# Kernel optimization log

Measured on AMD Instinct MI355X. Metric: run time of the kernel, lower is better.

Reference implementation:

```python
import jax, jax.numpy as jnp
import numpy as np

N, K, C0, H = 256, 16, 16, 32  # vertices, regular degree, input feats, hidden


def setup_inputs() -> dict:
    key = jax.random.key(0)
    ks = jax.random.split(key, 4)
    # k-regular circulant graph: neighbors of i are i+/-1..i+/-K//2 (mod N), sorted by vertex id
    offs = np.concatenate([np.arange(1, K // 2 + 1), -np.arange(1, K // 2 + 1)])
    nbrs = np.sort((np.arange(N)[:, None] + offs[None, :]) % N, axis=1).astype(np.int32)
    X = jax.random.normal(ks[0], (N, C0), jnp.float32)
    W1 = jax.random.normal(ks[1], (18 * C0, H), jnp.float32) / np.sqrt(18 * C0)
    b1 = jnp.zeros((H,), jnp.float32)
    W2 = jax.random.normal(ks[2], (18 * H, H), jnp.float32) / np.sqrt(18 * H)
    b2 = jnp.zeros((H,), jnp.float32)
    fc_w = jax.random.normal(ks[3], (H, 1), jnp.float32) / np.sqrt(H)
    fc_b = jnp.zeros((1,), jnp.float32)
    return {"X": X, "nbrs": jnp.asarray(nbrs), "W1": W1, "b1": b1,
            "W2": W2, "b2": b2, "fc_w": fc_w, "fc_b": fc_b}


def contract18(T, A):
    """All 18 contractions of F6[t,a,b,e,f,c] = T[t,a,b,c] * A[e,f],
    exactly matching _collapse6to3 (_c6to2_111 + _c6to2_12 + _c6to2_3),
    without materializing the 6-d tensor.
    T: (n, k, k, k, c) with axes (vertex, t, a, b, channel); A: (k, k).
    Returns (n, k, k, 18*c)."""
    S = A.sum()            # total sum of A
    r = A.sum(1)           # row sums
    tr = jnp.trace(A)
    sum_b = T.sum(3)              # (n,t,a,c)
    sum_t = T.sum(1)              # (n,a,b,c)
    sum_ab = T.sum((2, 3))        # (n,t,c)
    sum_tb = T.sum((1, 3))        # (n,a,c)
    sum_all = T.sum((1, 2, 3))    # (n,c)
    # _c6to2_111 (5 permutations)
    c1 = sum_b * S
    c2 = sum_ab[:, :, None, :] * r[None, None, :, None]
    c3 = sum_t * S
    c4 = sum_tb[:, :, None, :] * r[None, None, :, None]
    c5 = sum_all[:, None, None, :] * A[None, :, :, None]
    # _c6to2_12 (1 nontrivial permutation + 9 identical identity permutations)
    c6 = jnp.einsum('ntabc,b->ntac', T, r)
    c7 = sum_b * tr  # repeated 9 times, as in the source
    # _c6to2_3 (3 planar-diagonal contractions)
    d_ab = jnp.diagonal(T, axis1=2, axis2=3).transpose(0, 1, 3, 2)   # (n,t,a,c): T[t,a,a,c]
    c16 = jnp.einsum('ntac,ea->ntec', d_ab, A)
    d_tb = jnp.diagonal(T, axis1=1, axis2=3)                          # (n,a,c,t): T[t,a,t,c]
    c17 = jnp.einsum('nact,et->naec', d_tb, A)
    d_ttt = jnp.einsum('ntttc->ntc', T).sum(1)                        # (n,c)
    c18 = d_ttt[:, None, None, :] * A[None, :, :, None]
    return jnp.concatenate([c1, c2, c3, c4, c5, c6] + [c7] * 9 + [c16, c17, c18], axis=-1)


def _forward(X, nbrs, W1, b1, W2, b2, fc_w, fc_b):
    n, k = nbrs.shape
    # chi_{i,t}[a,p] = 1 iff a-th neighbor of i == p-th neighbor of j, j = nbrs[i,t]
    NN = nbrs[nbrs]                                                    # (n,k,k)
    CH = (nbrs[:, None, :, None] == NN[:, :, None, :]).astype(X.dtype)  # (n,t,a,p)
    A = jnp.eye(k, dtype=X.dtype)  # chi_{i,i} is the k x k identity for every i

    # get_F0: broadcast vertex features to (n, k, k, c0)
    F = jnp.broadcast_to(X[:, None, None, :], (n, k, k, X.shape[1]))

    def layer(F, W, b):
        Fg = F[nbrs]                                             # (n,t,p,q,c) gather neighbor features
        tmp = jnp.einsum('ntap,ntpqc->ntaqc', CH, Fg)            # chi @ F
        T = jnp.einsum('ntaqc,ntbq->ntabc', tmp, CH)             # (chi @ F) @ chi^T
        col = contract18(T, A)                                   # (n,k,k,18c)
        return jax.nn.relu(col @ W + b)

    F1 = layer(F, W1, b1)
    F2 = layer(F1, W2, b2)
    # get_Troot then full sum: chi_root scatters F2 entries injectively into [n,n,c],
    # so sum over Troot == sum over all entries of F2.
    g = F2.sum((0, 1, 2))                                        # (H,)
    return g @ fc_w + fc_b                                       # (1,)


def reference(X, nbrs, W1, b1, W2, b2, fc_w, fc_b):
    return _forward(X, nbrs, W1, b1, W2, b2, fc_w, fc_b)
```

## Files before the change

### kernel.cpp

```cpp
#include <hip/hip_runtime.h>


constexpr int KN = 16, HH = 32, NV = 256, C2 = 32;

typedef float f32x2 __attribute__((ext_vector_type(2)));
typedef float f32x4 __attribute__((ext_vector_type(4)));

__device__ __forceinline__ f32x2 pkfma(f32x2 a, f32x2 b, f32x2 c) {
    f32x2 d;
    asm("v_pk_fma_f32 %0, %1, %2, %3" : "=v"(d) : "v"(a), "v"(b), "v"(c));
    return d;
}
__device__ __forceinline__ f32x2 pkadd(f32x2 a, f32x2 b) {
    f32x2 d;
    asm("v_pk_add_f32 %0, %1, %2" : "=v"(d) : "v"(a), "v"(b));
    return d;
}
__device__ __forceinline__ f32x2 pkmul(f32x2 a, f32x2 b) {
    f32x2 d;
    asm("v_pk_mul_f32 %0, %1, %2" : "=v"(d) : "v"(a), "v"(b));
    return d;
}
__device__ __forceinline__ f32x2 vlo(f32x4 v) { return __builtin_shufflevector(v, v, 0, 1); }
__device__ __forceinline__ f32x2 vhi(f32x4 v) { return __builtin_shufflevector(v, v, 2, 3); }

#define MM_DS(WLDS, NC, COEF_EXPR, ACC2) do {                                  \
    const f32x4* W4_ = (const f32x4*)(WLDS);                                   \
    _Pragma("unroll")                                                          \
    for (int ci = 0; ci < (NC); ++ci) {                                        \
        const float cfs_ = (COEF_EXPR);                                        \
        const f32x2 cf2_ = {cfs_, cfs_};                                       \
        _Pragma("unroll")                                                      \
        for (int h4 = 0; h4 < 8; ++h4) {                                       \
            const f32x4 w_ = W4_[ci * 8 + h4];                                 \
            (ACC2)[2*h4+0] = pkfma(cf2_, vlo(w_), (ACC2)[2*h4+0]);             \
            (ACC2)[2*h4+1] = pkfma(cf2_, vhi(w_), (ACC2)[2*h4+1]);             \
        }                                                                      \
    }                                                                          \
} while (0)

__global__ __launch_bounds__(512)
void ccn_l1(const float* __restrict__ X, const int* __restrict__ nbrs,
            const float* __restrict__ W1, const float* __restrict__ bias,
            float* __restrict__ F1c, float* __restrict__ outz,
            const float* __restrict__ W2f, float* __restrict__ Wsb2)
{
    __shared__ float sE1[6 * 512];
    __shared__ float sPP2[8 * 256 * 4];
    __shared__ float sX[16][20];
    __shared__ float sV[16][164];
    __shared__ int   s_nbi[16];
    __shared__ int   s_nbj[16][17];
    __shared__ int   s_P[16][16];
    __shared__ int   s_vm[16];
    __shared__ float s_m[16];

    const int tid  = threadIdx.x;
    const int i    = ((blockIdx.x & 7) << 5) | (blockIdx.x >> 3);

    if (blockIdx.x == 0 && tid == 0) outz[0] = 0.f;

    if (blockIdx.x < 2) {
        const int u = (blockIdx.x << 9) | tid;
        float acc = 0.f;
        #pragma unroll
        for (int g = 6; g < 15; ++g) acc += W2f[g * 1024 + u];
        Wsb2[u] = 16.f * W2f[u] + W2f[5 * 1024 + u] + 16.f * acc;
    }

    if (tid < 16) s_nbi[tid] = nbrs[i * 16 + tid];
    __syncthreads();

    if (tid < 256) {
        const int t = tid >> 4, y = tid & 15;
        const int j = s_nbi[t];
        s_nbj[t][y] = nbrs[j * 16 + y];
        sX[t][y]    = X[j * 16 + y];
    } else {
        const int u = tid - 256;
        float acc = 0.f;
        #pragma unroll
        for (int g = 6; g < 15; ++g) acc += W1[g * 512 + u];
        sE1[u]        = 16.f * W1[u] + W1[5 * 512 + u] + 16.f * acc;
        sE1[512 + u]  = W1[512 + u];
        sE1[1024 + u] = W1[15 * 512 + u];
        sE1[1536 + u] = W1[2 * 512 + u];
        sE1[2048 + u] = W1[3 * 512 + u];
        sE1[2560 + u] = W1[4 * 512 + u];
    }
    __syncthreads();

    if (tid < 256) {
        const int t = tid >> 4, y = tid & 15;
        const int tgt = s_nbi[y];
        int p = -1;
        #pragma unroll
        for (int q = 0; q < 16; ++q) if (s_nbj[t][q] == tgt) p = q;
        s_P[t][y] = p;
        unsigned long long bal = __ballot(p >= 0);
        if (y == 0) {
            int vm = (int)((bal >> ((t & 3) * 16)) & 0xFFFFull);
            s_vm[t] = vm;
            s_m[t]  = (float)__popc(vm);
        }
    } else {
        const int u = tid;
        float acc = 0.f;
        #pragma unroll
        for (int g = 6; g < 15; ++g) acc += W1[g * 512 + u];
        sE1[u]        = 16.f * W1[u] + W1[5 * 512 + u] + 16.f * acc;
        sE1[512 + u]  = W1[512 + u];
        sE1[1024 + u] = W1[15 * 512 + u];
        sE1[1536 + u] = W1[2 * 512 + u];
        sE1[2048 + u] = W1[3 * 512 + u];
        sE1[2560 + u] = W1[4 * 512 + u];
    }
    __syncthreads();

    if (tid < 256) {
        const int t = tid >> 4, y = tid & 15, x = t;
        float Y0[16];
        #pragma unroll
        for (int c4 = 0; c4 < 4; ++c4) {
            float4 v = *(const float4*)&sX[t][4 * c4];
            Y0[4*c4+0] = v.x; Y0[4*c4+1] = v.y; Y0[4*c4+2] = v.z; Y0[4*c4+3] = v.w;
        }
        f32x2 Z42[8], Z52[8];
        #pragma unroll
        for (int c = 0; c < 8; ++c) { Z42[c] = (f32x2){0.f,0.f}; Z52[c] = (f32x2){0.f,0.f}; }
        #pragma unroll
        for (int tp = 0; tp < 16; ++tp) {
            const int vm = s_vm[tp];
            const float mt = s_m[tp];
            const float fb = ((vm >> x) & 1) ? mt : 0.f;
            const float f5 = mt * mt;
            const f32x2 fb2 = {fb, fb};
            const f32x2 f52 = {f5, f5};
            #pragma unroll
            for (int c4 = 0; c4 < 4; ++c4) {
                const f32x4 v = *(const f32x4*)&sX[tp][4 * c4];
                Z42[2*c4+0] = pkfma(fb2, vlo(v), Z42[2*c4+0]);
                Z42[2*c4+1] = pkfma(fb2, vhi(v), Z42[2*c4+1]);
                Z52[2*c4+0] = pkfma(f52, vlo(v), Z52[2*c4+0]);
                Z52[2*c4+1] = pkfma(f52, vhi(v), Z52[2*c4+1]);
            }
        }
        const float m = s_m[t];
        float v0a=0.f,v0b=0.f,v1a=0.f,v1b=0.f,v2a=0.f,v2b=0.f;
        float v3a=0.f,v3b=0.f,v4a=0.f,v4b=0.f;
        const float2* Wsb = (const float2*)(sE1 + 0 * 512);
        const float2* Wab = (const float2*)(sE1 + 1 * 512);
        const float2* W16 = (const float2*)(sE1 + 2 * 512);
        const float2* Wtb = (const float2*)(sE1 + 4 * 512);
        const float2* Wal = (const float2*)(sE1 + 5 * 512);
        #pragma unroll
        for (int c = 0; c < 16; ++c) {
            const float cf0 = m * Y0[c];
            const float cf1 = m * cf0;
            const float cf2 = Y0[c];
            const float cf3 = Z42[c >> 1][c & 1];
            const float cf4 = Z52[c >> 1][c & 1];
            const int idx = c * 16 + y;
            float2 w0 = Wsb[idx]; v0a = fmaf(cf0, w0.x, v0a); v0b = fmaf(cf0, w0.y, v0b);
            float2 w1 = Wab[idx]; v1a = fmaf(cf1, w1.x, v1a); v1b = fmaf(cf1, w1.y, v1b);
            float2 w2 = W16[idx]; v2a = fmaf(cf2, w2.x, v2a); v2b = fmaf(cf2, w2.y, v2b);
            float2 w3 = Wtb[idx]; v3a = fmaf(cf3, w3.x, v3a); v3b = fmaf(cf3, w3.y, v3b);
            float2 w4 = Wal[idx]; v4a = fmaf(cf4, w4.x, v4a); v4b = fmaf(cf4, w4.y, v4b);
        }
        *(float2*)&sV[t][0 * 32 + 2 * y] = make_float2(v0a, v0b);
        *(float2*)&sV[t][1 * 32 + 2 * y] = make_float2(v1a, v1b);
        *(float2*)&sV[t][2 * 32 + 2 * y] = make_float2(v2a, v2b);
        *(float2*)&sV[t][3 * 32 + 2 * y] = make_float2(v3a, v3b);
        *(float2*)&sV[t][4 * 32 + 2 * y] = make_float2(v4a, v4b);
    } else {
        const int w = tid - 256;
        const int t = w >> 4, y = w & 15, x = t;
        f32x2 Z22[8];
        #pragma unroll
        for (int c = 0; c < 8; ++c) Z22[c] = (f32x2){0.f,0.f};
        #pragma unroll
        for (int tp = 0; tp < 16; ++tp) {
            const int vm = s_vm[tp];
            const float f2 = (float)((vm >> x) & (vm >> y) & 1);
            const f32x2 f22 = {f2, f2};
            #pragma unroll
            for (int c4 = 0; c4 < 4; ++c4) {
                const f32x4 v = *(const f32x4*)&sX[tp][4 * c4];
                Z22[2*c4+0] = pkfma(f22, vlo(v), Z22[2*c4+0]);
                Z22[2*c4+1] = pkfma(f22, vhi(v), Z22[2*c4+1]);
            }
        }
        f32x2 pp2[16];
        #pragma unroll
        for (int h = 0; h < 16; ++h) pp2[h] = (f32x2){0.f,0.f};
        MM_DS(sE1 + 3 * 512, 16, 16.f * Z22[ci >> 1][ci & 1], pp2);
        const int cell = y * 16 + t;
        #pragma unroll
        for (int h4 = 0; h4 < 8; ++h4) {
            const int base = (h4 * 256 + cell) * 4;
            *(f32x2*)&sPP2[base]     = pp2[2*h4+0];
            *(f32x2*)&sPP2[base + 2] = pp2[2*h4+1];
        }
    }
    __syncthreads();

    if (tid < 256) {
        const int q = tid >> 4, p = tid & 15;
        const float vy  = (s_P[p][q] >= 0) ? 1.f : 0.f;
        const float dxy = (p == q) ? 1.f : 0.f;
        const f32x2 vy2 = {vy, vy}, dxy2 = {dxy, dxy};
        float4* F4 = (float4*)F1c;
        const size_t basec = ((size_t)i * 16 + q) * 128 + p;
        #pragma unroll
        for (int h4 = 0; h4 < 8; ++h4) {
            const f32x4 V0 = *(const f32x4*)&sV[p][0 * 32 + 4 * h4];
            const f32x4 V1 = *(const f32x4*)&sV[p][1 * 32 + 4 * h4];
            const f32x4 V2 = *(const f32x4*)&sV[p][2 * 32 + 4 * h4];
            const f32x4 V3 = *(const f32x4*)&sV[p][3 * 32 + 4 * h4];
            const f32x4 V4 = *(const f32x4*)&sV[p][4 * 32 + 4 * h4];
            const f32x4 PP = *(const f32x4*)&sPP2[(h4 * 256 + q * 16 + p) * 4];
            const f32x2 blo = *(const f32x2*)&bias[4 * h4];
            const f32x2 bhi = *(const f32x2*)&bias[4 * h4 + 2];
            f32x2 slo = pkadd(vlo(V0), vlo(V2));
            slo = pkfma(vy2, slo, vlo(V1));
            slo = pkadd(slo, vlo(V3));
            slo = pkfma(dxy2, vlo(V4), slo);
            slo = pkadd(slo, vlo(PP));
            slo = pkadd(slo, blo);
            f32x2 shi = pkadd(vhi(V0), vhi(V2));
            shi = pkfma(vy2, shi, vhi(V1));
            shi = pkadd(shi, vhi(V3));
            shi = pkfma(dxy2, vhi(V4), shi);
            shi = pkadd(shi, vhi(PP));
            shi = pkadd(shi, bhi);
            F4[basec + h4 * 16] = make_float4(fmaxf(slo.x, 0.f), fmaxf(slo.y, 0.f),
                                              fmaxf(shi.x, 0.f), fmaxf(shi.y, 0.f));
        }
    }
}

__global__ __launch_bounds__(512)
void ccn_l2(const float* __restrict__ F1c, const int* __restrict__ nbrs,
            const float* __restrict__ W2, const float* __restrict__ bias,
            const float* __restrict__ fcw, const float* __restrict__ fcb,
            float* __restrict__ out, const float* __restrict__ Wsb2)
{
    __shared__ float sMM[3 * 1024];
    __shared__ float sW3[3 * 1024];
    __shared__ float sRpp[256 * 36];
    __shared__ float s_stb[16 * 33];
    __shared__ float s_sall[C2];
    __shared__ int   s_nbi[16];
    __shared__ int   s_PQ[16 * 17];
    __shared__ float s_red[4];

    const int tid  = threadIdx.x;
    const int i    = ((blockIdx.x & 7) << 5) | (blockIdx.x >> 3);
    const int lane = tid & 63;
    const f32x4* F4 = (const f32x4*)F1c;

    if (tid < 16) s_nbi[tid] = nbrs[i * 16 + tid];
    __syncthreads();

    if (tid < 256) {
        const int t = tid >> 4, y = tid & 15;
        const int j = s_nbi[t];
        s_PQ[t * 17 + y] = nbrs[j * 16 + y];
    } else {
        const int w = tid - 256;
        ((f32x4*)sMM)[w]       = ((const f32x4*)Wsb2)[w];
        ((f32x4*)sMM)[256 + w] = ((const f32x4*)(W2 + 15 * 1024))[w];
        ((f32x4*)sMM)[512 + w] = ((const f32x4*)(W2 +  2 * 1024))[w];
        ((f32x4*)sW3)[w]       = ((const f32x4*)(W2 +  1 * 1024))[w];
        ((f32x4*)sW3)[256 + w] = ((const f32x4*)(W2 +  3 * 1024))[w];
        ((f32x4*)sW3)[512 + w] = ((const f32x4*)(W2 +  4 * 1024))[w];
    }
    __syncthreads();

    if (tid < 256) {
        const int t = tid >> 4, y = tid & 15;
        const int tgt = s_nbi[y];
        int p = -1;
        #pragma unroll
        for (int q = 0; q < 16; ++q) if (s_PQ[t * 17 + q] == tgt) p = q;
        s_PQ[t * 17 + y] = p;
    }
    __syncthreads();

    f32x2 pre2[16];
    float sab[C2];
    f32x2 pp2[16];

    if (tid < 256) {
        const int t = tid >> 4, y = tid & 15;
        const int j = s_nbi[t];
        const int p = s_PQ[t * 17 + y];
        const float mp = (p >= 0) ? 1.f : 0.f;
        const int pc = p >= 0 ? p : 0;
        const size_t jbase = (size_t)j * 2048;

        f32x2 R2[16];
        #pragma unroll
        for (int c = 0; c < 16; ++c) R2[c] = (f32x2){0.f, 0.f};
        #pragma unroll
        for (int b = 0; b < 16; ++b) {
            const int q = s_PQ[t * 17 + b];
            const float mm = (q >= 0) ? mp : 0.f;
            const f32x2 mm2 = {mm, mm};
            const int qc = q >= 0 ? q : 0;
            const size_t rb = jbase + (size_t)qc * 128 + pc;
            #pragma unroll
            for (int c4 = 0; c4 < 8; ++c4) {
                const f32x4 v = F4[rb + c4 * 16];
                R2[2*c4+0] = pkfma(mm2, vlo(v), R2[2*c4+0]);
                R2[2*c4+1] = pkfma(mm2, vhi(v), R2[2*c4+1]);
            }
        }
        {
            float* dst = &sRpp[(t * 16 + y) * 36];
            #pragma unroll
            for (int c4 = 0; c4 < 8; ++c4) {
                *(f32x2*)&dst[4*c4]     = R2[2*c4+0];
                *(f32x2*)&dst[4*c4 + 2] = R2[2*c4+1];
            }
        }

        #pragma unroll
        for (int h = 0; h < 16; ++h) pre2[h] = (f32x2){0.f, 0.f};
        MM_DS(sMM, 32, R2[ci >> 1][ci & 1], pre2);

        #pragma unroll
        for (int c = 0; c < C2; ++c) {
            float s = R2[c >> 1][c & 1];
            s += __shfl_xor(s, 1);
            s += __shfl_xor(s, 2);
            s += __shfl_xor(s, 4);
            s += __shfl_xor(s, 8);
            sab[c] = s;
        }

        f32x2 D2[16];
        {
            const f32x2 mp2 = {mp, mp};
            const size_t db = jbase + (size_t)pc * 128 + pc;
            #pragma unroll
            for (int c4 = 0; c4 < 8; ++c4) {
                const f32x4 v = F4[db + c4 * 16];
                D2[2*c4+0] = pkmul(mp2, vlo(v));
                D2[2*c4+1] = pkmul(mp2, vhi(v));
            }
        }
        MM_DS(sMM + 1024, 32, D2[ci >> 1][ci & 1], pre2);
    } else {
        const int w = tid - 256;
        const int g = w >> 4, l = w & 15;
        f32x2 ST2[16];
        #pragma unroll
        for (int c = 0; c < 16; ++c) ST2[c] = (f32x2){0.f, 0.f};
        #pragma unroll
        for (int tp = 0; tp < 16; ++tp) {
            const int jt = s_nbi[tp];
            const int py = s_PQ[tp * 17 + g];
            const int px = s_PQ[tp * 17 + l];
            const float mm = (px >= 0 && py >= 0) ? 1.f : 0.f;
            const f32x2 mm2 = {mm, mm};
            const int pyc = py >= 0 ? py : 0;
            const int pxc = px >= 0 ? px : 0;
            const size_t rb = (size_t)jt * 2048 + (size_t)pyc * 128 + pxc;
            #pragma unroll
            for (int c4 = 0; c4 < 8; ++c4) {
                const f32x4 v = F4[rb + c4 * 16];
                ST2[2*c4+0] = pkfma(mm2, vlo(v), ST2[2*c4+0]);
                ST2[2*c4+1] = pkfma(mm2, vhi(v), ST2[2*c4+1]);
            }
        }
        #pragma unroll
        for (int h = 0; h < 16; ++h) pp2[h] = (f32x2){0.f, 0.f};
        MM_DS(sMM + 2048, 32, 16.f * ST2[ci >> 1][ci & 1], pp2);
    }
    __syncthreads();

    if (tid < 256) {
        #pragma unroll
        for (int k = 0; k < 2; ++k) {
            const int x2 = (tid >> 5) + 8 * k;
            const int c = tid & 31;
            float s = 0.f;
            #pragma unroll
            for (int tt = 0; tt < 16; ++tt) s += sRpp[(tt * 16 + x2) * 36 + c];
            s_stb[x2 * 33 + c] = s;
        }
    }
    __syncthreads();

    if (tid < 256) {
        if (tid < 32) {
            float s = 0.f;
            #pragma unroll
            for (int x2 = 0; x2 < 16; ++x2) s += s_stb[x2 * 33 + tid];
            s_sall[tid] = s;
        }
    } else {
        const int w = tid - 256;
        const int g = w >> 4, l = w & 15;
        float* dst = &sRpp[(l * 16 + g) * 36];
        #pragma unroll
        for (int h4 = 0; h4 < 8; ++h4) {
            *(f32x2*)&dst[4*h4]     = pp2[2*h4+0];
            *(f32x2*)&dst[4*h4 + 2] = pp2[2*h4+1];
        }
    }
    __syncthreads();

    if (tid < 256) {
        const int t = tid >> 4, y = tid & 15, x = t;
        const float dxy = (x == y) ? 1.f : 0.f;
        float S0 = 0.f, S1 = 0.f, L0 = 0.f, L1 = 0.f;
        {
            const float2* Wab = (const float2*)(sW3 + 0 * 1024);
            const float2* Wtb = (const float2*)(sW3 + 1 * 1024);
            const float2* Wal = (const float2*)(sW3 + 2 * 1024);
            #pragma unroll
            for (int c = 0; c < C2; ++c) {
                const float cfa = sab[c];
                const float cft = s_stb[t * 33 + c];
                const float cfl = s_sall[c];
                const int idx = c * 16 + y;
                float2 wa = Wab[idx]; S0 = fmaf(cfa, wa.x, S0); S1 = fmaf(cfa, wa.y, S1);
                float2 wt = Wtb[idx]; S0 = fmaf(cft, wt.x, S0); S1 = fmaf(cft, wt.y, S1);
                float2 wl = Wal[idx]; L0 = fmaf(cfl, wl.x, L0); L1 = fmaf(cfl, wl.y, L1);
            }
        }
        const int gbase = (t & 3) * 16;
        #pragma unroll
        for (int h = 0; h < HH; ++h) {
            const int src = gbase + (h >> 1);
            const float sv = (h & 1) ? S1 : S0;
            const float lv = (h & 1) ? L1 : L0;
            pre2[h >> 1][h & 1] += __shfl(sv, src, 64) + dxy * __shfl(lv, src, 64);
        }
        {
            const float* ppr = &sRpp[(t * 16 + y) * 36];
            #pragma unroll
            for (int h4 = 0; h4 < 8; ++h4) {
                const f32x2 a = *(const f32x2*)&ppr[4*h4];
                const f32x2 b = *(const f32x2*)&ppr[4*h4 + 2];
                pre2[2*h4+0] = pkadd(pre2[2*h4+0], a);
                pre2[2*h4+1] = pkadd(pre2[2*h4+1], b);
            }
        }
        float local = 0.f;
        #pragma unroll
        for (int h = 0; h < HH; ++h) {
            float v = pre2[h >> 1][h & 1] + bias[h];
            v = v > 0.f ? v : 0.f;
            local += v * fcw[h];
        }
        #pragma unroll
        for (int off = 32; off > 0; off >>= 1) local += __shfl_down(local, off, 64);
        if (lane == 0) s_red[tid >> 6] = local;
    }
    __syncthreads();
    if (tid == 0) {
        const float v = s_red[0] + s_red[1] + s_red[2] + s_red[3]
                      + fcb[0] * (1.f / 256.f);
        atomicAdd(out, v);
    }
}

extern "C" void kernel_launch(void* const* d_in, const int* in_sizes, int n_in,
                              void* d_out, int out_size, void* d_ws, size_t ws_size,
                              hipStream_t stream) {
    const float* X    = (const float*)d_in[0];
    const int*   nbrs = (const int*)  d_in[1];
    const float* W1   = (const float*)d_in[2];
    const float* b1   = (const float*)d_in[3];
    const float* W2   = (const float*)d_in[4];
    const float* b2   = (const float*)d_in[5];
    const float* fc_w = (const float*)d_in[6];
    const float* fc_b = (const float*)d_in[7];
    float* outp = (float*)d_out;

    float* F1c  = (float*)d_ws;
    float* Wsb2 = F1c + 2097152;

    ccn_l1<<<NV, 512, 0, stream>>>(X, nbrs, W1, b1, F1c, outp, W2, Wsb2);
    ccn_l2<<<NV, 512, 0, stream>>>(F1c, nbrs, W2, b2, fc_w, fc_b, outp, Wsb2);
}
```

Before: 104.6 us.

## Use op_sel packed FMAs for broadcast coefficients and split reductions across thread halves

Adds packed-FMA variants that use op_sel to broadcast one lane of a coefficient pair, so matrix-multiply loops consume coefficient pairs directly instead of building splatted vectors. Layer 1 precomputes the Z4/Z5 neighbour sums once into shared memory with separate threads, instead of each thread recomputing them. In layer 2 the per-channel sab sums move from a wave-shuffle reduction to a shared-memory tree reduction done by the otherwise idle upper half of the block. Shared-memory row strides change from 36/33 to 34. The cost is an extra barrier and more shared memory, and the 34-float stride may cause more bank conflicts than the old padding.

```diff
diff --git a/kernel.cpp b/kernel.cpp
--- a/kernel.cpp
+++ b/kernel.cpp
@@ -11,6 +11,18 @@
     asm("v_pk_fma_f32 %0, %1, %2, %3" : "=v"(d) : "v"(a), "v"(b), "v"(c));
     return d;
 }
+__device__ __forceinline__ f32x2 pkfma_lo(f32x2 cf, f32x2 w, f32x2 acc) {
+    f32x2 d;
+    asm("v_pk_fma_f32 %0, %1, %2, %3 op_sel:[0,0,0] op_sel_hi:[0,1,1]"
+        : "=v"(d) : "v"(cf), "v"(w), "v"(acc));
+    return d;
+}
+__device__ __forceinline__ f32x2 pkfma_hi(f32x2 cf, f32x2 w, f32x2 acc) {
+    f32x2 d;
+    asm("v_pk_fma_f32 %0, %1, %2, %3 op_sel:[1,0,0] op_sel_hi:[1,1,1]"
+        : "=v"(d) : "v"(cf), "v"(w), "v"(acc));
+    return d;
+}
 __device__ __forceinline__ f32x2 pkadd(f32x2 a, f32x2 b) {
     f32x2 d;
     asm("v_pk_add_f32 %0, %1, %2" : "=v"(d) : "v"(a), "v"(b));
@@ -24,17 +36,22 @@
 __device__ __forceinline__ f32x2 vlo(f32x4 v) { return __builtin_shufflevector(v, v, 0, 1); }
 __device__ __forceinline__ f32x2 vhi(f32x4 v) { return __builtin_shufflevector(v, v, 2, 3); }
 
-#define MM_DS(WLDS, NC, COEF_EXPR, ACC2) do {                                  \
+#define MM_DSP(WLDS, NC2, CPARR, ACC2) do {                                    \
     const f32x4* W4_ = (const f32x4*)(WLDS);                                   \
     _Pragma("unroll")                                                          \
-    for (int ci = 0; ci < (NC); ++ci) {                                        \
-        const float cfs_ = (COEF_EXPR);                                        \
-        const f32x2 cf2_ = {cfs_, cfs_};                                       \
+    for (int cp = 0; cp < (NC2); ++cp) {                                       \
+        const f32x2 cfp_ = (CPARR)[cp];                                        \
         _Pragma("unroll")                                                      \
         for (int h4 = 0; h4 < 8; ++h4) {                                       \
-            const f32x4 w_ = W4_[ci * 8 + h4];                                 \
-            (ACC2)[2*h4+0] = pkfma(cf2_, vlo(w_), (ACC2)[2*h4+0]);             \
-            (ACC2)[2*h4+1] = pkfma(cf2_, vhi(w_), (ACC2)[2*h4+1]);             \
+            const f32x4 w_ = W4_[(2 * cp) * 8 + h4];                           \
+            (ACC2)[2*h4+0] = pkfma_lo(cfp_, vlo(w_), (ACC2)[2*h4+0]);          \
+            (ACC2)[2*h4+1] = pkfma_lo(cfp_, vhi(w_), (ACC2)[2*h4+1]);          \
+        }                                                                      \
+        _Pragma("unroll")                                                      \
+        for (int h4 = 0; h4 < 8; ++h4) {                                       \
+            const f32x4 w_ = W4_[(2 * cp + 1) * 8 + h4];                       \
+            (ACC2)[2*h4+0] = pkfma_hi(cfp_, vlo(w_), (ACC2)[2*h4+0]);          \
+            (ACC2)[2*h4+1] = pkfma_hi(cfp_, vhi(w_), (ACC2)[2*h4+1]);          \
         }                                                                      \
     }                                                                          \
 } while (0)
@@ -49,6 +66,8 @@
     __shared__ float sPP2[8 * 256 * 4];
     __shared__ float sX[16][20];
     __shared__ float sV[16][164];
+    __shared__ float s_Z4[16][20];
+    __shared__ float s_Z5[16];
     __shared__ int   s_nbi[16];
     __shared__ int   s_nbj[16][17];
     __shared__ int   s_P[16][16];
@@ -118,60 +137,68 @@
     __syncthreads();
 
     if (tid < 256) {
-        const int t = tid >> 4, y = tid & 15, x = t;
-        float Y0[16];
+        const int t = tid >> 4, c = tid & 15;
+        float acc = 0.f;
+        #pragma unroll
+        for (int tp = 0; tp < 16; ++tp) {
+            const float fb = ((s_vm[tp] >> t) & 1) ? s_m[tp] : 0.f;
+            acc = fmaf(fb, sX[tp][c], acc);
+        }
+        s_Z4[t][c] = acc;
+    } else if (tid < 272) {
+        const int c = tid - 256;
+        float acc = 0.f;
+        #pragma unroll
+        for (int tp = 0; tp < 16; ++tp) {
+            const float mt = s_m[tp];
+            acc = fmaf(mt * mt, sX[tp][c], acc);
+        }
+        s_Z5[c] = acc;
+    }
+    __syncthreads();
+
+    if (tid < 256) {
+        const int t = tid >> 4, y = tid & 15;
+        f32x2 Y0p[8];
         #pragma unroll
         for (int c4 = 0; c4 < 4; ++c4) {
-            float4 v = *(const float4*)&sX[t][4 * c4];
-            Y0[4*c4+0] = v.x; Y0[4*c4+1] = v.y; Y0[4*c4+2] = v.z; Y0[4*c4+3] = v.w;
-        }
-        f32x2 Z42[8], Z52[8];
-        #pragma unroll
-        for (int c = 0; c < 8; ++c) { Z42[c] = (f32x2){0.f,0.f}; Z52[c] = (f32x2){0.f,0.f}; }
-        #pragma unroll
-        for (int tp = 0; tp < 16; ++tp) {
-            const int vm = s_vm[tp];
-            const float mt = s_m[tp];
-            const float fb = ((vm >> x) & 1) ? mt : 0.f;
-            const float f5 = mt * mt;
-            const f32x2 fb2 = {fb, fb};
-            const f32x2 f52 = {f5, f5};
-            #pragma unroll
-            for (int c4 = 0; c4 < 4; ++c4) {
-                const f32x4 v = *(const f32x4*)&sX[tp][4 * c4];
-                Z42[2*c4+0] = pkfma(fb2, vlo(v), Z42[2*c4+0]);
-                Z42[2*c4+1] = pkfma(fb2, vhi(v), Z42[2*c4+1]);
-                Z52[2*c4+0] = pkfma(f52, vlo(v), Z52[2*c4+0]);
-                Z52[2*c4+1] = pkfma(f52, vhi(v), Z52[2*c4+1]);
-            }
+            const f32x4 v = *(const f32x4*)&sX[t][4 * c4];
+            Y0p[2*c4+0] = vlo(v); Y0p[2*c4+1] = vhi(v);
         }
         const float m = s_m[t];
-        float v0a=0.f,v0b=0.f,v1a=0.f,v1b=0.f,v2a=0.f,v2b=0.f;
-        float v3a=0.f,v3b=0.f,v4a=0.f,v4b=0.f;
+        const f32x2 mp2 = {m, m};
+        f32x2 v0p = {0.f,0.f}, v1p = {0.f,0.f}, v2p = {0.f,0.f};
+        f32x2 v3p = {0.f,0.f}, v4p = {0.f,0.f};
         const float2* Wsb = (const float2*)(sE1 + 0 * 512);
         const float2* Wab = (const float2*)(sE1 + 1 * 512);
         const float2* W16 = (const float2*)(sE1 + 2 * 512);
         const float2* Wtb = (const float2*)(sE1 + 4 * 512);
         const float2* Wal = (const float2*)(sE1 + 5 * 512);
         #pragma unroll
-        for (int c = 0; c < 16; ++c) {
-            const float cf0 = m * Y0[c];
-            const float cf1 = m * cf0;
-            const float cf2 = Y0[c];
-            const float cf3 = Z42[c >> 1][c & 1];
-            const float cf4 = Z52[c >> 1][c & 1];
-            const int idx = c * 16 + y;
-            float2 w0 = Wsb[idx]; v0a = fmaf(cf0, w0.x, v0a); v0b = fmaf(cf0, w0.y, v0b);
-            float2 w1 = Wab[idx]; v1a = fmaf(cf1, w1.x, v1a); v1b = fmaf(cf1, w1.y, v1b);
-            float2 w2 = W16[idx]; v2a = fmaf(cf2, w2.x, v2a); v2b = fmaf(cf2, w2.y, v2b);
-            float2 w3 = Wtb[idx]; v3a = fmaf(cf3, w3.x, v3a); v3b = fmaf(cf3, w3.y, v3b);
-            float2 w4 = Wal[idx]; v4a = fmaf(cf4, w4.x, v4a); v4b = fmaf(cf4, w4.y, v4b);
-        }
-        *(float2*)&sV[t][0 * 32 + 2 * y] = make_float2(v0a, v0b);
-        *(float2*)&sV[t][1 * 32 + 2 * y] = make_float2(v1a, v1b);
-        *(float2*)&sV[t][2 * 32 + 2 * y] = make_float2(v2a, v2b);
-        *(float2*)&sV[t][3 * 32 + 2 * y] = make_float2(v3a, v3b);
-        *(float2*)&sV[t][4 * 32 + 2 * y] = make_float2(v4a, v4b);
+        for (int cp = 0; cp < 8; ++cp) {
+            const f32x2 cf0p = pkmul(mp2, Y0p[cp]);
+            const f32x2 cf1p = pkmul(mp2, cf0p);
+            const f32x2 cf2p = Y0p[cp];
+            const f32x2 cf3p = *(const f32x2*)&s_Z4[t][2 * cp];
+            const f32x2 cf4p = *(const f32x2*)&s_Z5[2 * cp];
+            const int i0 = (2 * cp) * 16 + y, i1 = (2 * cp + 1) * 16 + y;
+            f32x2 w;
+            w = *(const f32x2*)&Wsb[i0]; v0p = pkfma_lo(cf0p, w, v0p);
+            w = *(const f32x2*)&Wsb[i1]; v0p = pkfma_hi(cf0p, w, v0p);
+            w = *(const f32x2*)&Wab[i0]; v1p = pkfma_lo(cf1p, w, v1p);
+            w = *(const f32x2*)&Wab[i1]; v1p = pkfma_hi(cf1p, w, v1p);
+            w = *(const f32x2*)&W16[i0]; v2p = pkfma_lo(cf2p, w, v2p);
+            w = *(const f32x2*)&W16[i1]; v2p = pkfma_hi(cf2p, w, v2p);
+            w = *(const f32x2*)&Wtb[i0]; v3p = pkfma_lo(cf3p, w, v3p);
+            w = *(const f32x2*)&Wtb[i1]; v3p = pkfma_hi(cf3p, w, v3p);
+            w = *(const f32x2*)&Wal[i0]; v4p = pkfma_lo(cf4p, w, v4p);
+            w = *(const f32x2*)&Wal[i1]; v4p = pkfma_hi(cf4p, w, v4p);
+        }
+        *(f32x2*)&sV[t][0 * 32 + 2 * y] = v0p;
+        *(f32x2*)&sV[t][1 * 32 + 2 * y] = v1p;
+        *(f32x2*)&sV[t][2 * 32 + 2 * y] = v2p;
+        *(f32x2*)&sV[t][3 * 32 + 2 * y] = v3p;
+        *(f32x2*)&sV[t][4 * 32 + 2 * y] = v4p;
     } else {
         const int w = tid - 256;
         const int t = w >> 4, y = w & 15, x = t;
@@ -190,10 +217,14 @@
                 Z22[2*c4+1] = pkfma(f22, vhi(v), Z22[2*c4+1]);
             }
         }
+        f32x2 Z22s[8];
+        const f32x2 sixteen = {16.f, 16.f};
+        #pragma unroll
+        for (int k = 0; k < 8; ++k) Z22s[k] = pkmul(sixteen, Z22[k]);
         f32x2 pp2[16];
         #pragma unroll
         for (int h = 0; h < 16; ++h) pp2[h] = (f32x2){0.f,0.f};
-        MM_DS(sE1 + 3 * 512, 16, 16.f * Z22[ci >> 1][ci & 1], pp2);
+        MM_DSP(sE1 + 3 * 512, 8, Z22s, pp2);
         const int cell = y * 16 + t;
         #pragma unroll
         for (int h4 = 0; h4 < 8; ++h4) {
@@ -247,8 +278,9 @@
 {
     __shared__ float sMM[3 * 1024];
     __shared__ float sW3[3 * 1024];
-    __shared__ float sRpp[256 * 36];
-    __shared__ float s_stb[16 * 33];
+    __shared__ float sRpp[256 * 34];
+    __shared__ float s_stb[16 * 34];
+    __shared__ float s_sab[16 * 34];
     __shared__ float s_sall[C2];
     __shared__ int   s_nbi[16];
     __shared__ int   s_PQ[16 * 17];
@@ -288,7 +320,6 @@
     __syncthreads();
 
     f32x2 pre2[16];
-    float sab[C2];
     f32x2 pp2[16];
 
     if (tid < 256) {
@@ -317,7 +348,7 @@
             }
         }
         {
-            float* dst = &sRpp[(t * 16 + y) * 36];
+            float* dst = &sRpp[(t * 16 + y) * 34];
             #pragma unroll
             for (int c4 = 0; c4 < 8; ++c4) {
                 *(f32x2*)&dst[4*c4]     = R2[2*c4+0];
@@ -327,17 +358,7 @@
 
         #pragma unroll
         for (int h = 0; h < 16; ++h) pre2[h] = (f32x2){0.f, 0.f};
-        MM_DS(sMM, 32, R2[ci >> 1][ci & 1], pre2);
-
-        #pragma unroll
-        for (int c = 0; c < C2; ++c) {
-            float s = R2[c >> 1][c & 1];
-            s += __shfl_xor(s, 1);
-            s += __shfl_xor(s, 2);
-            s += __shfl_xor(s, 4);
-            s += __shfl_xor(s, 8);
-            sab[c] = s;
-        }
+        MM_DSP(sMM, 16, R2, pre2);
 
         f32x2 D2[16];
         {
@@ -350,7 +371,7 @@
                 D2[2*c4+1] = pkmul(mp2, vhi(v));
             }
         }
-        MM_DS(sMM + 1024, 32, D2[ci >> 1][ci & 1], pre2);
+        MM_DSP(sMM + 1024, 16, D2, pre2);
     } else {
         const int w = tid - 256;
         const int g = w >> 4, l = w & 15;
@@ -374,9 +395,13 @@
                 ST2[2*c4+1] = pkfma(mm2, vhi(v), ST2[2*c4+1]);
             }
         }
+        f32x2 ST2s[16];
+        const f32x2 sixteen = {16.f, 16.f};
+        #pragma unroll
+        for (int k = 0; k < 16; ++k) ST2s[k] = pkmul(sixteen, ST2[k]);
         #pragma unroll
         for (int h = 0; h < 16; ++h) pp2[h] = (f32x2){0.f, 0.f};
-        MM_DS(sMM + 2048, 32, 16.f * ST2[ci >> 1][ci & 1], pp2);
+        MM_DSP(sMM + 2048, 16, ST2s, pp2);
     }
     __syncthreads();
 
@@ -387,9 +412,24 @@
             const int c = tid & 31;
             float s = 0.f;
             #pragma unroll
-            for (int tt = 0; tt < 16; ++tt) s += sRpp[(tt * 16 + x2) * 36 + c];
-            s_stb[x2 * 33 + c] = s;
-        }
+            for (int tt = 0; tt < 16; ++tt) s += sRpp[(tt * 16 + x2) * 34 + c];
+            s_stb[x2 * 34 + c] = s;
+        }
+    } else {
+        const int w = tid - 256;
+        const int t = w >> 4, cp = w & 15;
+        f32x2 v[16];
+        #pragma unroll
+        for (int yy = 0; yy < 16; ++yy)
+            v[yy] = *(const f32x2*)&sRpp[(t * 16 + yy) * 34 + 2 * cp];
+        f32x2 t1[8], t2[4], t3[2];
+        #pragma unroll
+        for (int k = 0; k < 8; ++k) t1[k] = pkadd(v[2*k], v[2*k+1]);
+        #pragma unroll
+        for (int k = 0; k < 4; ++k) t2[k] = pkadd(t1[2*k], t1[2*k+1]);
+        #pragma unroll
+        for (int k = 0; k < 2; ++k) t3[k] = pkadd(t2[2*k], t2[2*k+1]);
+        *(f32x2*)&s_sab[t * 34 + 2 * cp] = pkadd(t3[0], t3[1]);
     }
     __syncthreads();
 
@@ -397,13 +437,13 @@
         if (tid < 32) {
             float s = 0.f;
             #pragma unroll
-            for (int x2 = 0; x2 < 16; ++x2) s += s_stb[x2 * 33 + tid];
+            for (int x2 = 0; x2 < 16; ++x2) s += s_stb[x2 * 34 + tid];
             s_sall[tid] = s;
         }
     } else {
         const int w = tid - 256;
         const int g = w >> 4, l = w & 15;
-        float* dst = &sRpp[(l * 16 + g) * 36];
+        float* dst = &sRpp[(l * 16 + g) * 34];
         #pragma unroll
         for (int h4 = 0; h4 < 8; ++h4) {
             *(f32x2*)&dst[4*h4]     = pp2[2*h4+0];
@@ -415,22 +455,27 @@
     if (tid < 256) {
         const int t = tid >> 4, y = tid & 15, x = t;
         const float dxy = (x == y) ? 1.f : 0.f;
-        float S0 = 0.f, S1 = 0.f, L0 = 0.f, L1 = 0.f;
+        f32x2 Sp = {0.f, 0.f}, Lp = {0.f, 0.f};
         {
             const float2* Wab = (const float2*)(sW3 + 0 * 1024);
             const float2* Wtb = (const float2*)(sW3 + 1 * 1024);
             const float2* Wal = (const float2*)(sW3 + 2 * 1024);
             #pragma unroll
-            for (int c = 0; c < C2; ++c) {
-                const float cfa = sab[c];
-                const float cft = s_stb[t * 33 + c];
-                const float cfl = s_sall[c];
-                const int idx = c * 16 + y;
-                float2 wa = Wab[idx]; S0 = fmaf(cfa, wa.x, S0); S1 = fmaf(cfa, wa.y, S1);
-                float2 wt = Wtb[idx]; S0 = fmaf(cft, wt.x, S0); S1 = fmaf(cft, wt.y, S1);
-                float2 wl = Wal[idx]; L0 = fmaf(cfl, wl.x, L0); L1 = fmaf(cfl, wl.y, L1);
-            }
-        }
+            for (int cp = 0; cp < 16; ++cp) {
+                const f32x2 cfap = *(const f32x2*)&s_sab[t * 34 + 2 * cp];
+                const f32x2 cftp = *(const f32x2*)&s_stb[t * 34 + 2 * cp];
+                const f32x2 cflp = *(const f32x2*)&s_sall[2 * cp];
+                const int i0 = (2 * cp) * 16 + y, i1 = (2 * cp + 1) * 16 + y;
+                f32x2 w;
+                w = *(const f32x2*)&Wab[i0]; Sp = pkfma_lo(cfap, w, Sp);
+                w = *(const f32x2*)&Wtb[i0]; Sp = pkfma_lo(cftp, w, Sp);
+                w = *(const f32x2*)&Wab[i1]; Sp = pkfma_hi(cfap, w, Sp);
+                w = *(const f32x2*)&Wtb[i1]; Sp = pkfma_hi(cftp, w, Sp);
+                w = *(const f32x2*)&Wal[i0]; Lp = pkfma_lo(cflp, w, Lp);
+                w = *(const f32x2*)&Wal[i1]; Lp = pkfma_hi(cflp, w, Lp);
+            }
+        }
+        const float S0 = Sp.x, S1 = Sp.y, L0 = Lp.x, L1 = Lp.y;
         const int gbase = (t & 3) * 16;
         #pragma unroll
         for (int h = 0; h < HH; ++h) {
@@ -440,7 +485,7 @@
             pre2[h >> 1][h & 1] += __shfl(sv, src, 64) + dxy * __shfl(lv, src, 64);
         }
         {
-            const float* ppr = &sRpp[(t * 16 + y) * 36];
+            const float* ppr = &sRpp[(t * 16 + y) * 34];
             #pragma unroll
             for (int h4 = 0; h4 < 8; ++h4) {
                 const f32x2 a = *(const f32x2*)&ppr[4*h4];
```

After: 105.7 us. Within noise of the previous version (+1.1%).
